# Kernel optimization log

Hardware: AMD Instinct MI355X
Metric: run time of the kernel (lower is better)

The kernel has to match this reference:

```python
import jax, jax.numpy as jnp
import numpy as np

EMB = 1024
HID = 1536
NE = 8


def setup_inputs() -> dict:
    key = jax.random.key(0)
    ks = jax.random.split(key, 8)
    B, N, E, H, ne = 4, 2048, EMB, HID, NE
    s = 1.0 / np.sqrt(E)
    sh = 1.0 / np.sqrt(H)
    return {
        "x": jax.random.normal(ks[0], (B, N, E), dtype=jnp.float32),
        "Wr": jax.random.uniform(ks[1], (E, ne), minval=-s, maxval=s, dtype=jnp.float32),
        "br": jax.random.uniform(ks[2], (ne,), minval=-s, maxval=s, dtype=jnp.float32),
        "W1": jax.random.uniform(ks[3], (ne, E, H), minval=-s, maxval=s, dtype=jnp.float32),
        "b1": jax.random.uniform(ks[4], (ne, H), minval=-s, maxval=s, dtype=jnp.float32),
        "W2": jax.random.uniform(ks[5], (ne, H, E), minval=-sh, maxval=sh, dtype=jnp.float32),
        "b2": jax.random.uniform(ks[6], (ne, E), minval=-sh, maxval=sh, dtype=jnp.float32),
        "k": 2,
    }


def reference(x, Wr, br, W1, b1, W2, b2, k):
    B, N, E = x.shape
    T = B * N
    ne = Wr.shape[1]
    flat = x.reshape(T, E)
    logits = flat @ Wr + br                      # [T, ne]
    _, topk_idx = jax.lax.top_k(logits, k)       # [T, k]
    # counts[t, e] = number of top-k slots of token t assigned to expert e
    counts = jax.nn.one_hot(topk_idx, ne, dtype=flat.dtype).sum(axis=1)  # [T, ne]
    out = jnp.zeros_like(flat)
    for e in range(ne):  # small fixed loop over experts (structurally distinct weights)
        h = jax.nn.gelu(flat @ W1[e] + b1[e], approximate=False)  # torch nn.GELU = exact erf
        y = h @ W2[e] + b2[e]
        out = out + counts[:, e:e + 1] * y
    out = out / k
    return out.reshape(B, N, E)
```

## Files before the change

kernel.cpp:

```cpp
#include <hip/hip_runtime.h>
#include <hip/hip_bf16.h>
#include <math.h>

#define T_TOK 8192
#define EMB   1024
#define HID   1536
#define NE    8
#define NBINB 64
#define BINTOK (T_TOK / NBINB)

typedef float  floatx4 __attribute__((ext_vector_type(4)));
typedef __bf16 bf16x8  __attribute__((ext_vector_type(8)));

#define WS_COUNTS   0
#define WS_OFFSETS  1024
#define WS_FLAGS    2048
#define WS_BHIST    4096
#define WS_TOKMAP   8192
#define WS_TOKLIST  270336
#define WS_YBUF     532480
#define WS_W1T      34086912
#define WS_W2T      59252736
#define WS_H        84418560
#define WS_NEEDED   135143424

__device__ __forceinline__ float eload(const void* p, size_t idx, bool f32) {
  return f32 ? ((const float*)p)[idx] : (float)(((const __bf16*)p)[idx]);
}

__device__ __forceinline__ void glds16(const void* g, void* l) {
  __builtin_amdgcn_global_load_lds(
      (const __attribute__((address_space(1))) unsigned int*)g,
      (__attribute__((address_space(3))) unsigned int*)l, 16, 0, 0);
}

__global__ __launch_bounds__(256)
void sniff_kernel(const void* p0, const void* p1, const void* p2, const void* p3,
                  const void* p4, const void* p5, const void* p6, int* flags) {
  const void* ps[7] = {p0, p1, p2, p3, p4, p5, p6};
  const int nelem[7] = {T_TOK * EMB, EMB * NE, NE, NE * EMB * HID, NE * HID, NE * HID * EMB, NE * EMB};
  int t = blockIdx.x;
  const unsigned* w = (const unsigned*)ps[t];
  int nw = nelem[t] / 2;
  if (nw > 2048) nw = 2048;
  __shared__ int s_pl, s_nz;
  if (threadIdx.x == 0) { s_pl = 0; s_nz = 0; }
  __syncthreads();
  int pl = 0, nz = 0;
  for (int i = threadIdx.x; i < nw; i += 256) {
    unsigned v = w[i];
    if (v == 0) continue;
    nz++;
    unsigned e = (v >> 23) & 0xFF;
    if (e >= 100 && e <= 150) pl++;
  }
  atomicAdd(&s_pl, pl);
  atomicAdd(&s_nz, nz);
  __syncthreads();
  if (threadIdx.x == 0) flags[t] = (2 * s_pl > s_nz) ? 1 : 0;
}

__global__ __launch_bounds__(256)
void logits_kernel(const void* __restrict__ x, const void* __restrict__ Wr,
                   const void* __restrict__ br, const int* __restrict__ kptr,
                   const int* __restrict__ flags, int* __restrict__ topk,
                   __bf16* __restrict__ xbf) {
  const bool xf32  = flags[0] != 0;
  const bool wrf32 = flags[1] != 0;
  const bool brf32 = flags[2] != 0;
  const int wave = threadIdx.x >> 6;
  const int lane = threadIdx.x & 63;
  const int t = blockIdx.x * 4 + wave;

  float xv[16];
  {
    size_t base = (size_t)t * EMB + lane * 16;
    if (xf32) {
      const float* g = (const float*)x + base;
#pragma unroll
      for (int j = 0; j < 16; ++j) xv[j] = g[j];
    } else {
      bf16x8 u = *(const bf16x8*)((const __bf16*)x + base);
      bf16x8 v = *(const bf16x8*)((const __bf16*)x + base + 8);
#pragma unroll
      for (int j = 0; j < 8; ++j) { xv[j] = (float)u[j]; xv[8 + j] = (float)v[j]; }
    }
  }
  {
    bf16x8 o0, o1;
#pragma unroll
    for (int j = 0; j < 8; ++j) { o0[j] = (__bf16)xv[j]; o1[j] = (__bf16)xv[8 + j]; }
    __bf16* xo = xbf + (size_t)t * EMB + lane * 16;
    *(bf16x8*)xo = o0;
    *(bf16x8*)(xo + 8) = o1;
  }
  float acc[NE];
#pragma unroll
  for (int e = 0; e < NE; ++e) acc[e] = 0.f;
  if (wrf32) {
#pragma unroll
    for (int j = 0; j < 16; ++j) {
      const float* wr = (const float*)Wr + (size_t)(lane * 16 + j) * NE;
#pragma unroll
      for (int e = 0; e < NE; ++e) acc[e] += xv[j] * wr[e];
    }
  } else {
#pragma unroll
    for (int j = 0; j < 16; ++j) {
      bf16x8 wr = *(const bf16x8*)((const __bf16*)Wr + (size_t)(lane * 16 + j) * NE);
#pragma unroll
      for (int e = 0; e < NE; ++e) acc[e] += xv[j] * (float)wr[e];
    }
  }
#pragma unroll
  for (int e = 0; e < NE; ++e) {
#pragma unroll
    for (int off = 32; off > 0; off >>= 1)
      acc[e] += __shfl_xor(acc[e], off, 64);
  }
  if (lane == 0) {
    int k = kptr[0];
    if (k < 1) k = 1; if (k > NE) k = NE;
    float lg[NE];
#pragma unroll
    for (int e = 0; e < NE; ++e) lg[e] = acc[e] + eload(br, e, brf32);
    for (int s = 0; s < k; ++s) {
      int bi = 0; float bv = lg[0];
#pragma unroll
      for (int e = 1; e < NE; ++e) { if (lg[e] > bv) { bv = lg[e]; bi = e; } }
      lg[bi] = -3.0e38f;
      topk[t * 8 + s] = bi;
    }
  }
}

__global__ __launch_bounds__(128)
void bin1_kernel(const int* __restrict__ topk, const int* __restrict__ kptr,
                 int* __restrict__ bhist) {
  __shared__ int lhist[NE];
  if (threadIdx.x < NE) lhist[threadIdx.x] = 0;
  __syncthreads();
  int k = kptr[0];
  if (k < 1) k = 1; if (k > NE) k = NE;
  const int t = blockIdx.x * BINTOK + threadIdx.x;
  for (int s = 0; s < k; ++s) atomicAdd(&lhist[topk[t * 8 + s] & 7], 1);
  __syncthreads();
  if (threadIdx.x < NE) bhist[blockIdx.x * NE + threadIdx.x] = lhist[threadIdx.x];
}

__global__ __launch_bounds__(256)
void scan_kernel(int* __restrict__ bhist, int* __restrict__ counts, int* __restrict__ offsets) {
  __shared__ int sh[NBINB * NE];
  __shared__ int scnt[NE];
  __shared__ int soff[NE + 1];
  const int tid = threadIdx.x;
  for (int i = tid; i < NBINB * NE; i += 256) sh[i] = bhist[i];
  __syncthreads();
  if (tid < NE) {
    int s = 0;
    for (int b = 0; b < NBINB; ++b) s += sh[b * NE + tid];
    scnt[tid] = s;
  }
  __syncthreads();
  if (tid == 0) {
    int s = 0;
    for (int e = 0; e < NE; ++e) { soff[e] = s; s += scnt[e]; }
    soff[NE] = s;
  }
  __syncthreads();
  if (tid < NE) {
    int run = soff[tid];
    for (int b = 0; b < NBINB; ++b) {
      int v = sh[b * NE + tid];
      sh[b * NE + tid] = run;
      run += v;
    }
  }
  __syncthreads();
  for (int i = tid; i < NBINB * NE; i += 256) bhist[i] = sh[i];
  if (tid < NE) counts[tid] = scnt[tid];
  if (tid < NE + 1) offsets[tid] = soff[tid];
}

__global__ __launch_bounds__(128)
void bin2_kernel(const int* __restrict__ bhist, const int* __restrict__ offsets,
                 const int* __restrict__ kptr,
                 int* __restrict__ tok_list, int* __restrict__ tokmap) {
  __shared__ int lbase[NE];
  __shared__ int lcnt[NE];
  if (threadIdx.x < NE) {
    lbase[threadIdx.x] = bhist[blockIdx.x * NE + threadIdx.x];
    lcnt[threadIdx.x] = 0;
  }
  __syncthreads();
  int k = kptr[0];
  if (k < 1) k = 1; if (k > NE) k = NE;
  const int t = blockIdx.x * BINTOK + threadIdx.x;
  for (int s = 0; s < k; ++s) {
    int e = tokmap[t * 8 + s] & 7;
    int pos = atomicAdd(&lcnt[e], 1);
    int grow = lbase[e] + pos;
    tok_list[e * T_TOK + (grow - offsets[e])] = t;
    tokmap[t * 8 + s] = (e << 16) | grow;
  }
}

__global__ __launch_bounds__(256)
void transpose2_kernel(const void* __restrict__ W1, const void* __restrict__ W2,
                       __bf16* __restrict__ w1t, __bf16* __restrict__ w2t,
                       const int* __restrict__ flags) {
  const int z = blockIdx.z;
  const void* in; __bf16* out; int K, N; bool f32;
  if (z < 8) { in = W1; out = w1t; K = EMB; N = HID; f32 = flags[3] != 0; }
  else       { in = W2; out = w2t; K = HID; N = EMB; f32 = flags[5] != 0; }
  if ((int)blockIdx.x * 64 >= N || (int)blockIdx.y * 64 >= K) return;
  __shared__ __bf16 tile[64][66];
  size_t eoff = (size_t)(z & 7) * (size_t)K * (size_t)N;
  const int n0 = blockIdx.x * 64;
  const int k0 = blockIdx.y * 64;
  const int tid = threadIdx.x;

  if (f32) {
    const int nn = (tid & 15) * 4;
    const int kr = tid >> 4;
#pragma unroll
    for (int p = 0; p < 4; ++p) {
      const int k = kr + p * 16;
      float4 v = *(const float4*)((const float*)in + eoff + (size_t)(k0 + k) * N + n0 + nn);
      tile[k][nn + 0] = (__bf16)v.x; tile[k][nn + 1] = (__bf16)v.y;
      tile[k][nn + 2] = (__bf16)v.z; tile[k][nn + 3] = (__bf16)v.w;
    }
  } else {
    const int nn = (tid & 7) * 8;
    const int kr = tid >> 3;
#pragma unroll
    for (int p = 0; p < 2; ++p) {
      const int k = kr + p * 32;
      bf16x8 v = *(const bf16x8*)((const __bf16*)in + eoff + (size_t)(k0 + k) * N + n0 + nn);
#pragma unroll
      for (int j = 0; j < 8; ++j) tile[k][nn + j] = v[j];
    }
  }
  __syncthreads();
  const int kk = (tid & 7) * 8;
  const int nr = tid >> 3;
#pragma unroll
  for (int p = 0; p < 2; ++p) {
    const int n = nr + p * 32;
    bf16x8 o;
#pragma unroll
    for (int j = 0; j < 8; ++j) o[j] = tile[kk + j][n];
    *(bf16x8*)(out + eoff + (size_t)(n0 + n) * K + k0 + kk) = o;
  }
}


__global__ __launch_bounds__(256, 4)
void gemm1_kernel(const __bf16* __restrict__ xbf, const __bf16* __restrict__ w1t,
                  const void* __restrict__ b1, const int* __restrict__ counts,
                  const int* __restrict__ offsets, const int* __restrict__ tok_list,
                  const int* __restrict__ flags, __bf16* __restrict__ hbuf) {
  const int flat = blockIdx.x;
  const int e   = flat & 7;
  const int idx = flat >> 3;
  const int g   = idx / 12;
  const int nT  = idx % 12;
  const int cnt = counts[e];
  const bool b1f32 = flags[4] != 0;

  __shared__ __align__(16) __bf16 As[128 * 64];
  __shared__ __align__(16) __bf16 Bs[128 * 64];

  const int wave = threadIdx.x >> 6;
  const int lane = threadIdx.x & 63;
  const int lrow = lane >> 3;
  const int cgs  = (lane & 7) ^ lrow;

  int Rst[4];
#pragma unroll
  for (int q = 0; q < 4; ++q) Rst[q] = (q * 4 + wave) * 8 + lrow;

  const __bf16* pB[4];
#pragma unroll
  for (int q = 0; q < 4; ++q)
    pB[q] = w1t + ((size_t)e * HID + nT * 128 + Rst[q]) * EMB + cgs * 8;

  const int wm = (wave & 1) * 64;
  const int wn = (wave >> 1) * 64;
  const int fr = lane & 15;
  const int fc = lane >> 4;
  int aOff0[4], aOff1[4], bOff0[4], bOff1[4];
#pragma unroll
  for (int i = 0; i < 4; ++i) {
    int R = wm + i * 16 + fr;
    aOff0[i] = R * 128 + (((fc)     ^ (R & 7)) << 4);
    aOff1[i] = R * 128 + (((fc + 4) ^ (R & 7)) << 4);
  }
#pragma unroll
  for (int j = 0; j < 4; ++j) {
    int R = wn + j * 16 + fr;
    bOff0[j] = R * 128 + (((fc)     ^ (R & 7)) << 4);
    bOff1[j] = R * 128 + (((fc + 4) ^ (R & 7)) << 4);
  }

  const int colBase = nT * 128 + wn + fr;
  float bv[4];
#pragma unroll
  for (int j = 0; j < 4; ++j) bv[j] = eload(b1, (size_t)e * HID + colBase + j * 16, b1f32);

  for (int mT = g; mT * 128 < cnt; mT += 16) {
    const __bf16* pA[4];
#pragma unroll
    for (int q = 0; q < 4; ++q) {
      const int tok = tok_list[e * T_TOK + mT * 128 + Rst[q]];
      pA[q] = xbf + (size_t)tok * EMB + cgs * 8;
    }

    floatx4 acc[4][4];
#pragma unroll
    for (int i = 0; i < 4; ++i)
#pragma unroll
      for (int j = 0; j < 4; ++j) acc[i][j] = (floatx4){0.f, 0.f, 0.f, 0.f};

    for (int kb = 0; kb < EMB / 64; ++kb) {
      __syncthreads();
#pragma unroll
      for (int q = 0; q < 4; ++q) glds16(pA[q] + (size_t)kb * 64, As + (q * 4 + wave) * 512);
#pragma unroll
      for (int q = 0; q < 4; ++q) glds16(pB[q] + (size_t)kb * 64, Bs + (q * 4 + wave) * 512);
      __syncthreads();
      bf16x8 af[4], bfr[4];
#pragma unroll
      for (int i = 0; i < 4; ++i) af[i]  = *(const bf16x8*)((const char*)As + aOff0[i]);
#pragma unroll
      for (int j = 0; j < 4; ++j) bfr[j] = *(const bf16x8*)((const char*)Bs + bOff0[j]);
#pragma unroll
      for (int i = 0; i < 4; ++i)
#pragma unroll
        for (int j = 0; j < 4; ++j)
          acc[i][j] = __builtin_amdgcn_mfma_f32_16x16x32_bf16(af[i], bfr[j], acc[i][j], 0, 0, 0);
#pragma unroll
      for (int i = 0; i < 4; ++i) af[i]  = *(const bf16x8*)((const char*)As + aOff1[i]);
#pragma unroll
      for (int j = 0; j < 4; ++j) bfr[j] = *(const bf16x8*)((const char*)Bs + bOff1[j]);
#pragma unroll
      for (int i = 0; i < 4; ++i)
#pragma unroll
        for (int j = 0; j < 4; ++j)
          acc[i][j] = __builtin_amdgcn_mfma_f32_16x16x32_bf16(af[i], bfr[j], acc[i][j], 0, 0, 0);
    }

    const int hBase = offsets[e] + mT * 128;
#pragma unroll
    for (int i = 0; i < 4; ++i) {
      const int rowLoc = wm + i * 16 + fc * 4;
#pragma unroll
      for (int r = 0; r < 4; ++r) {
        const int row = rowLoc + r;
        if (mT * 128 + row < cnt) {
          __bf16* hp = hbuf + (size_t)(hBase + row) * HID + colBase;
#pragma unroll
          for (int j = 0; j < 4; ++j) {
            float v = acc[i][j][r] + bv[j];
            float gl = 0.5f * v * (1.0f + erff(v * 0.70710678118654752f));
            hp[j * 16] = (__bf16)gl;
          }
        }
      }
    }
  }
}

__global__ __launch_bounds__(256, 4)
void gemm2_kernel(const __bf16* __restrict__ hbuf, const __bf16* __restrict__ w2t,
                  const void* __restrict__ b2, const int* __restrict__ counts,
                  const int* __restrict__ offsets, const int* __restrict__ flags,
                  __bf16* __restrict__ ybuf) {
  const int flat = blockIdx.x;
  const int e   = flat & 7;
  const int idx = flat >> 3;
  const int g   = idx >> 3;
  const int nT  = idx & 7;
  const int cnt = counts[e];
  const bool b2f32 = flags[6] != 0;

  __shared__ __align__(16) __bf16 As[128 * 64];
  __shared__ __align__(16) __bf16 Bs[128 * 64];

  const int wave = threadIdx.x >> 6;
  const int lane = threadIdx.x & 63;
  const int lrow = lane >> 3;
  const int cgs  = (lane & 7) ^ lrow;

  int Rst[4];
#pragma unroll
  for (int q = 0; q < 4; ++q) Rst[q] = (q * 4 + wave) * 8 + lrow;

  const __bf16* pB[4];
#pragma unroll
  for (int q = 0; q < 4; ++q)
    pB[q] = w2t + ((size_t)e * EMB + nT * 128 + Rst[q]) * HID + cgs * 8;

  const int wm = (wave & 1) * 64;
  const int wn = (wave >> 1) * 64;
  const int fr = lane & 15;
  const int fc = lane >> 4;
  int aOff0[4], aOff1[4], bOff0[4], bOff1[4];
#pragma unroll
  for (int i = 0; i < 4; ++i) {
    int R = wm + i * 16 + fr;
    aOff0[i] = R * 128 + (((fc)     ^ (R & 7)) << 4);
    aOff1[i] = R * 128 + (((fc + 4) ^ (R & 7)) << 4);
  }
#pragma unroll
  for (int j = 0; j < 4; ++j) {
    int R = wn + j * 16 + fr;
    bOff0[j] = R * 128 + (((fc)     ^ (R & 7)) << 4);
    bOff1[j] = R * 128 + (((fc + 4) ^ (R & 7)) << 4);
  }

  const int colBase = nT * 128 + wn + fr;
  float bv[4];
#pragma unroll
  for (int j = 0; j < 4; ++j) bv[j] = eload(b2, (size_t)e * EMB + colBase + j * 16, b2f32);

  for (int mT = g; mT * 128 < cnt; mT += 16) {
    const int rowBase = offsets[e] + mT * 128;
    const __bf16* pA[4];
#pragma unroll
    for (int q = 0; q < 4; ++q)
      pA[q] = hbuf + (size_t)(rowBase + Rst[q]) * HID + cgs * 8;

    floatx4 acc[4][4];
#pragma unroll
    for (int i = 0; i < 4; ++i)
#pragma unroll
      for (int j = 0; j < 4; ++j) acc[i][j] = (floatx4){0.f, 0.f, 0.f, 0.f};

    for (int kb = 0; kb < HID / 64; ++kb) {
      __syncthreads();
#pragma unroll
      for (int q = 0; q < 4; ++q) glds16(pA[q] + (size_t)kb * 64, As + (q * 4 + wave) * 512);
#pragma unroll
      for (int q = 0; q < 4; ++q) glds16(pB[q] + (size_t)kb * 64, Bs + (q * 4 + wave) * 512);
      __syncthreads();
      bf16x8 af[4], bfr[4];
#pragma unroll
      for (int i = 0; i < 4; ++i) af[i]  = *(const bf16x8*)((const char*)As + aOff0[i]);
#pragma unroll
      for (int j = 0; j < 4; ++j) bfr[j] = *(const bf16x8*)((const char*)Bs + bOff0[j]);
#pragma unroll
      for (int i = 0; i < 4; ++i)
#pragma unroll
        for (int j = 0; j < 4; ++j)
          acc[i][j] = __builtin_amdgcn_mfma_f32_16x16x32_bf16(af[i], bfr[j], acc[i][j], 0, 0, 0);
#pragma unroll
      for (int i = 0; i < 4; ++i) af[i]  = *(const bf16x8*)((const char*)As + aOff1[i]);
#pragma unroll
      for (int j = 0; j < 4; ++j) bfr[j] = *(const bf16x8*)((const char*)Bs + bOff1[j]);
#pragma unroll
      for (int i = 0; i < 4; ++i)
#pragma unroll
        for (int j = 0; j < 4; ++j)
          acc[i][j] = __builtin_amdgcn_mfma_f32_16x16x32_bf16(af[i], bfr[j], acc[i][j], 0, 0, 0);
    }

#pragma unroll
    for (int i = 0; i < 4; ++i) {
      const int rowLoc = wm + i * 16 + fc * 4;
#pragma unroll
      for (int r = 0; r < 4; ++r) {
        const int row = rowLoc + r;
        if (mT * 128 + row < cnt) {
          __bf16* yp = ybuf + (size_t)(rowBase + row) * EMB + colBase;
#pragma unroll
          for (int j = 0; j < 4; ++j)
            yp[j * 16] = (__bf16)(acc[i][j][r] + bv[j]);
        }
      }
    }
  }
}

__global__ __launch_bounds__(256)
void combine_kernel(const __bf16* __restrict__ ybuf, const int* __restrict__ tokmap,
                    const int* __restrict__ kptr, const int* __restrict__ flags,
                    void* __restrict__ out) {
  const bool f32 = flags[0] != 0;
  const int wave = threadIdx.x >> 6;
  const int lane = threadIdx.x & 63;
  const int t = blockIdx.x * 4 + wave;
  int k = kptr[0];
  if (k < 1) k = 1; if (k > NE) k = NE;
  const float invk = 1.0f / (float)k;
  int rows[NE];
  for (int s = 0; s < k; ++s) rows[s] = tokmap[t * 8 + s] & 0xFFFF;
#pragma unroll
  for (int c = 0; c < 2; ++c) {
    const int i = c * 512 + lane * 8;
    float a[8];
#pragma unroll
    for (int j = 0; j < 8; ++j) a[j] = 0.f;
    for (int s = 0; s < k; ++s) {
      bf16x8 y = *(const bf16x8*)(ybuf + (size_t)rows[s] * EMB + i);
#pragma unroll
      for (int j = 0; j < 8; ++j) a[j] += (float)y[j];
    }
    if (f32) {
      float* op = (float*)out + (size_t)t * EMB + i;
      float4 u = {a[0] * invk, a[1] * invk, a[2] * invk, a[3] * invk};
      float4 v = {a[4] * invk, a[5] * invk, a[6] * invk, a[7] * invk};
      *(float4*)op = u;
      *(float4*)(op + 4) = v;
    } else {
      bf16x8 o;
#pragma unroll
      for (int j = 0; j < 8; ++j) o[j] = (__bf16)(a[j] * invk);
      *(bf16x8*)((__bf16*)out + (size_t)t * EMB + i) = o;
    }
  }
}

extern "C" void kernel_launch(void* const* d_in, const int* in_sizes, int n_in,
                              void* d_out, int out_size, void* d_ws, size_t ws_size,
                              hipStream_t stream) {
  (void)in_sizes; (void)n_in; (void)out_size;
  if (ws_size < (size_t)WS_NEEDED) return;

  const void* x  = d_in[0];
  const void* Wr = d_in[1];
  const void* br = d_in[2];
  const void* W1 = d_in[3];
  const void* b1 = d_in[4];
  const void* W2 = d_in[5];
  const void* b2 = d_in[6];
  const int* kptr = (const int*)d_in[7];

  char* ws = (char*)d_ws;
  int*    counts   = (int*)(ws + WS_COUNTS);
  int*    offsets  = (int*)(ws + WS_OFFSETS);
  int*    flags    = (int*)(ws + WS_FLAGS);
  int*    bhist    = (int*)(ws + WS_BHIST);
  int*    tokmap   = (int*)(ws + WS_TOKMAP);
  int*    tok_list = (int*)(ws + WS_TOKLIST);
  __bf16* ybuf     = (__bf16*)(ws + WS_YBUF);
  __bf16* xbf      = (__bf16*)(ws + WS_YBUF);
  __bf16* w1t      = (__bf16*)(ws + WS_W1T);
  __bf16* w2t      = (__bf16*)(ws + WS_W2T);
  __bf16* hbuf     = (__bf16*)(ws + WS_H);

  hipMemsetAsync(ws + WS_TOKLIST, 0, NE * T_TOK * 4, stream);

  sniff_kernel<<<dim3(7), 256, 0, stream>>>(x, Wr, br, W1, b1, W2, b2, flags);

  transpose2_kernel<<<dim3(HID / 64, HID / 64, 16), 256, 0, stream>>>(W1, W2, w1t, w2t, flags);

  logits_kernel<<<dim3(T_TOK / 4), 256, 0, stream>>>(x, Wr, br, kptr, flags, tokmap, xbf);
  bin1_kernel<<<dim3(NBINB), 128, 0, stream>>>(tokmap, kptr, bhist);
  scan_kernel<<<dim3(1), 256, 0, stream>>>(bhist, counts, offsets);
  bin2_kernel<<<dim3(NBINB), 128, 0, stream>>>(bhist, offsets, kptr, tok_list, tokmap);

  gemm1_kernel<<<dim3(8 * 16 * 12), 256, 0, stream>>>(
      xbf, w1t, b1, counts, offsets, tok_list, flags, hbuf);
  gemm2_kernel<<<dim3(8 * 16 * 8), 256, 0, stream>>>(
      hbuf, w2t, b2, counts, offsets, flags, ybuf);

  combine_kernel<<<dim3(T_TOK / 4), 256, 0, stream>>>(ybuf, tokmap, kptr, flags, d_out);
}
```

Before: 368.5 us.

## Fuse weight transpose with logits, collapse binning into one single-block kernel

Merges the weight transpose/convert kernel and the router logits kernel into one launch partitioned by block index. The three binning kernels (histogram, scan, scatter) and the memset become a single 1024-thread block that assigns per-expert positions directly and zero-pads only the tail of each expert list. Combine now adds the expert offset to recover global rows. It also vectorizes the fp32 x load. This cuts launch count and removes the transpose-to-logits serialization, but binning on one block is serial over 8192 tokens and the atomic order makes slot assignment nondeterministic.

```diff
diff --git a/kernel.cpp b/kernel.cpp
--- a/kernel.cpp
+++ b/kernel.cpp
@@ -6,8 +6,6 @@
 #define EMB   1024
 #define HID   1536
 #define NE    8
-#define NBINB 64
-#define BINTOK (T_TOK / NBINB)
 
 typedef float  floatx4 __attribute__((ext_vector_type(4)));
 typedef __bf16 bf16x8  __attribute__((ext_vector_type(8)));
@@ -15,7 +13,6 @@
 #define WS_COUNTS   0
 #define WS_OFFSETS  1024
 #define WS_FLAGS    2048
-#define WS_BHIST    4096
 #define WS_TOKMAP   8192
 #define WS_TOKLIST  270336
 #define WS_YBUF     532480
@@ -61,16 +58,70 @@
 }
 
 __global__ __launch_bounds__(256)
-void logits_kernel(const void* __restrict__ x, const void* __restrict__ Wr,
-                   const void* __restrict__ br, const int* __restrict__ kptr,
-                   const int* __restrict__ flags, int* __restrict__ topk,
-                   __bf16* __restrict__ xbf) {
+void prep_kernel(const void* __restrict__ W1, const void* __restrict__ W2,
+                 __bf16* __restrict__ w1t, __bf16* __restrict__ w2t,
+                 const void* __restrict__ x, const void* __restrict__ Wr,
+                 const void* __restrict__ br, const int* __restrict__ kptr,
+                 const int* __restrict__ flags, int* __restrict__ topk,
+                 __bf16* __restrict__ xbf) {
+  __shared__ __bf16 tile[64][66];
+  const int bid = blockIdx.x;
+  const int tid = threadIdx.x;
+
+  if (bid < 6144) {
+    const void* in; __bf16* out; int K, N; bool f32; int e, nb, kb;
+    if (bid < 3072) {
+      in = W1; out = w1t; K = EMB; N = HID; f32 = flags[3] != 0;
+      e = bid / 384; int rem = bid % 384; nb = rem % 24; kb = rem / 24;
+    } else {
+      in = W2; out = w2t; K = HID; N = EMB; f32 = flags[5] != 0;
+      int w = bid - 3072; e = w / 384; int rem = w % 384; nb = rem % 16; kb = rem / 16;
+    }
+    size_t eoff = (size_t)e * (size_t)K * (size_t)N;
+    const int n0 = nb * 64;
+    const int k0 = kb * 64;
+
+    if (f32) {
+      const int nn = (tid & 15) * 4;
+      const int kr = tid >> 4;
+#pragma unroll
+      for (int p = 0; p < 4; ++p) {
+        const int k = kr + p * 16;
+        float4 v = *(const float4*)((const float*)in + eoff + (size_t)(k0 + k) * N + n0 + nn);
+        tile[k][nn + 0] = (__bf16)v.x; tile[k][nn + 1] = (__bf16)v.y;
+        tile[k][nn + 2] = (__bf16)v.z; tile[k][nn + 3] = (__bf16)v.w;
+      }
+    } else {
+      const int nn = (tid & 7) * 8;
+      const int kr = tid >> 3;
+#pragma unroll
+      for (int p = 0; p < 2; ++p) {
+        const int k = kr + p * 32;
+        bf16x8 v = *(const bf16x8*)((const __bf16*)in + eoff + (size_t)(k0 + k) * N + n0 + nn);
+#pragma unroll
+        for (int j = 0; j < 8; ++j) tile[k][nn + j] = v[j];
+      }
+    }
+    __syncthreads();
+    const int kk = (tid & 7) * 8;
+    const int nr = tid >> 3;
+#pragma unroll
+    for (int p = 0; p < 2; ++p) {
+      const int n = nr + p * 32;
+      bf16x8 o;
+#pragma unroll
+      for (int j = 0; j < 8; ++j) o[j] = tile[kk + j][n];
+      *(bf16x8*)(out + eoff + (size_t)(n0 + n) * K + k0 + kk) = o;
+    }
+    return;
+  }
+
   const bool xf32  = flags[0] != 0;
   const bool wrf32 = flags[1] != 0;
   const bool brf32 = flags[2] != 0;
-  const int wave = threadIdx.x >> 6;
-  const int lane = threadIdx.x & 63;
-  const int t = blockIdx.x * 4 + wave;
+  const int wave = tid >> 6;
+  const int lane = tid & 63;
+  const int t = (bid - 6144) * 4 + wave;
 
   float xv[16];
   {
@@ -78,7 +129,10 @@
     if (xf32) {
       const float* g = (const float*)x + base;
 #pragma unroll
-      for (int j = 0; j < 16; ++j) xv[j] = g[j];
+      for (int c = 0; c < 4; ++c) {
+        float4 v = *(const float4*)(g + c * 4);
+        xv[c * 4 + 0] = v.x; xv[c * 4 + 1] = v.y; xv[c * 4 + 2] = v.z; xv[c * 4 + 3] = v.w;
+      }
     } else {
       bf16x8 u = *(const bf16x8*)((const __bf16*)x + base);
       bf16x8 v = *(const bf16x8*)((const __bf16*)x + base + 8);
@@ -134,123 +188,38 @@
   }
 }
 
-__global__ __launch_bounds__(128)
-void bin1_kernel(const int* __restrict__ topk, const int* __restrict__ kptr,
-                 int* __restrict__ bhist) {
-  __shared__ int lhist[NE];
-  if (threadIdx.x < NE) lhist[threadIdx.x] = 0;
+__global__ __launch_bounds__(1024)
+void bin_kernel(const int* __restrict__ kptr, int* __restrict__ tokmap,
+                int* __restrict__ tok_list, int* __restrict__ counts,
+                int* __restrict__ offsets) {
+  __shared__ int lcnt[NE];
+  __shared__ int soff[NE + 1];
+  const int tid = threadIdx.x;
+  if (tid < NE) lcnt[tid] = 0;
   __syncthreads();
   int k = kptr[0];
   if (k < 1) k = 1; if (k > NE) k = NE;
-  const int t = blockIdx.x * BINTOK + threadIdx.x;
-  for (int s = 0; s < k; ++s) atomicAdd(&lhist[topk[t * 8 + s] & 7], 1);
-  __syncthreads();
-  if (threadIdx.x < NE) bhist[blockIdx.x * NE + threadIdx.x] = lhist[threadIdx.x];
-}
-
-__global__ __launch_bounds__(256)
-void scan_kernel(int* __restrict__ bhist, int* __restrict__ counts, int* __restrict__ offsets) {
-  __shared__ int sh[NBINB * NE];
-  __shared__ int scnt[NE];
-  __shared__ int soff[NE + 1];
-  const int tid = threadIdx.x;
-  for (int i = tid; i < NBINB * NE; i += 256) sh[i] = bhist[i];
-  __syncthreads();
-  if (tid < NE) {
-    int s = 0;
-    for (int b = 0; b < NBINB; ++b) s += sh[b * NE + tid];
-    scnt[tid] = s;
+  for (int t = tid; t < T_TOK; t += 1024) {
+    for (int s = 0; s < k; ++s) {
+      int e = tokmap[t * 8 + s] & 7;
+      int pos = atomicAdd(&lcnt[e], 1);
+      tok_list[e * T_TOK + pos] = t;
+      tokmap[t * 8 + s] = (e << 16) | pos;
+    }
   }
   __syncthreads();
   if (tid == 0) {
     int s = 0;
-    for (int e = 0; e < NE; ++e) { soff[e] = s; s += scnt[e]; }
+    for (int e = 0; e < NE; ++e) { soff[e] = s; s += lcnt[e]; }
     soff[NE] = s;
   }
   __syncthreads();
-  if (tid < NE) {
-    int run = soff[tid];
-    for (int b = 0; b < NBINB; ++b) {
-      int v = sh[b * NE + tid];
-      sh[b * NE + tid] = run;
-      run += v;
-    }
-  }
-  __syncthreads();
-  for (int i = tid; i < NBINB * NE; i += 256) bhist[i] = sh[i];
-  if (tid < NE) counts[tid] = scnt[tid];
-  if (tid < NE + 1) offsets[tid] = soff[tid];
-}
-
-__global__ __launch_bounds__(128)
-void bin2_kernel(const int* __restrict__ bhist, const int* __restrict__ offsets,
-                 const int* __restrict__ kptr,
-                 int* __restrict__ tok_list, int* __restrict__ tokmap) {
-  __shared__ int lbase[NE];
-  __shared__ int lcnt[NE];
-  if (threadIdx.x < NE) {
-    lbase[threadIdx.x] = bhist[blockIdx.x * NE + threadIdx.x];
-    lcnt[threadIdx.x] = 0;
-  }
-  __syncthreads();
-  int k = kptr[0];
-  if (k < 1) k = 1; if (k > NE) k = NE;
-  const int t = blockIdx.x * BINTOK + threadIdx.x;
-  for (int s = 0; s < k; ++s) {
-    int e = tokmap[t * 8 + s] & 7;
-    int pos = atomicAdd(&lcnt[e], 1);
-    int grow = lbase[e] + pos;
-    tok_list[e * T_TOK + (grow - offsets[e])] = t;
-    tokmap[t * 8 + s] = (e << 16) | grow;
-  }
-}
-
-__global__ __launch_bounds__(256)
-void transpose2_kernel(const void* __restrict__ W1, const void* __restrict__ W2,
-                       __bf16* __restrict__ w1t, __bf16* __restrict__ w2t,
-                       const int* __restrict__ flags) {
-  const int z = blockIdx.z;
-  const void* in; __bf16* out; int K, N; bool f32;
-  if (z < 8) { in = W1; out = w1t; K = EMB; N = HID; f32 = flags[3] != 0; }
-  else       { in = W2; out = w2t; K = HID; N = EMB; f32 = flags[5] != 0; }
-  if ((int)blockIdx.x * 64 >= N || (int)blockIdx.y * 64 >= K) return;
-  __shared__ __bf16 tile[64][66];
-  size_t eoff = (size_t)(z & 7) * (size_t)K * (size_t)N;
-  const int n0 = blockIdx.x * 64;
-  const int k0 = blockIdx.y * 64;
-  const int tid = threadIdx.x;
-
-  if (f32) {
-    const int nn = (tid & 15) * 4;
-    const int kr = tid >> 4;
-#pragma unroll
-    for (int p = 0; p < 4; ++p) {
-      const int k = kr + p * 16;
-      float4 v = *(const float4*)((const float*)in + eoff + (size_t)(k0 + k) * N + n0 + nn);
-      tile[k][nn + 0] = (__bf16)v.x; tile[k][nn + 1] = (__bf16)v.y;
-      tile[k][nn + 2] = (__bf16)v.z; tile[k][nn + 3] = (__bf16)v.w;
-    }
-  } else {
-    const int nn = (tid & 7) * 8;
-    const int kr = tid >> 3;
-#pragma unroll
-    for (int p = 0; p < 2; ++p) {
-      const int k = kr + p * 32;
-      bf16x8 v = *(const bf16x8*)((const __bf16*)in + eoff + (size_t)(k0 + k) * N + n0 + nn);
-#pragma unroll
-      for (int j = 0; j < 8; ++j) tile[k][nn + j] = v[j];
-    }
-  }
-  __syncthreads();
-  const int kk = (tid & 7) * 8;
-  const int nr = tid >> 3;
-#pragma unroll
-  for (int p = 0; p < 2; ++p) {
-    const int n = nr + p * 32;
-    bf16x8 o;
-#pragma unroll
-    for (int j = 0; j < 8; ++j) o[j] = tile[kk + j][n];
-    *(bf16x8*)(out + eoff + (size_t)(n0 + n) * K + k0 + kk) = o;
+  if (tid < NE) counts[tid] = lcnt[tid];
+  if (tid <= NE) offsets[tid] = soff[tid];
+  for (int e = 0; e < NE; ++e) {
+    const int c = lcnt[e];
+    const int end = (c + 127) & ~127;
+    for (int i = c + tid; i < end; i += 1024) tok_list[e * T_TOK + i] = 0;
   }
 }
 
@@ -484,8 +453,8 @@
 
 __global__ __launch_bounds__(256)
 void combine_kernel(const __bf16* __restrict__ ybuf, const int* __restrict__ tokmap,
-                    const int* __restrict__ kptr, const int* __restrict__ flags,
-                    void* __restrict__ out) {
+                    const int* __restrict__ offsets, const int* __restrict__ kptr,
+                    const int* __restrict__ flags, void* __restrict__ out) {
   const bool f32 = flags[0] != 0;
   const int wave = threadIdx.x >> 6;
   const int lane = threadIdx.x & 63;
@@ -494,7 +463,10 @@
   if (k < 1) k = 1; if (k > NE) k = NE;
   const float invk = 1.0f / (float)k;
   int rows[NE];
-  for (int s = 0; s < k; ++s) rows[s] = tokmap[t * 8 + s] & 0xFFFF;
+  for (int s = 0; s < k; ++s) {
+    int m = tokmap[t * 8 + s];
+    rows[s] = offsets[(m >> 16) & 7] + (m & 0xFFFF);
+  }
 #pragma unroll
   for (int c = 0; c < 2; ++c) {
     const int i = c * 512 + lane * 8;
@@ -540,7 +512,6 @@
   int*    counts   = (int*)(ws + WS_COUNTS);
   int*    offsets  = (int*)(ws + WS_OFFSETS);
   int*    flags    = (int*)(ws + WS_FLAGS);
-  int*    bhist    = (int*)(ws + WS_BHIST);
   int*    tokmap   = (int*)(ws + WS_TOKMAP);
   int*    tok_list = (int*)(ws + WS_TOKLIST);
   __bf16* ybuf     = (__bf16*)(ws + WS_YBUF);
@@ -549,21 +520,17 @@
   __bf16* w2t      = (__bf16*)(ws + WS_W2T);
   __bf16* hbuf     = (__bf16*)(ws + WS_H);
 
-  hipMemsetAsync(ws + WS_TOKLIST, 0, NE * T_TOK * 4, stream);
-
   sniff_kernel<<<dim3(7), 256, 0, stream>>>(x, Wr, br, W1, b1, W2, b2, flags);
 
-  transpose2_kernel<<<dim3(HID / 64, HID / 64, 16), 256, 0, stream>>>(W1, W2, w1t, w2t, flags);
-
-  logits_kernel<<<dim3(T_TOK / 4), 256, 0, stream>>>(x, Wr, br, kptr, flags, tokmap, xbf);
-  bin1_kernel<<<dim3(NBINB), 128, 0, stream>>>(tokmap, kptr, bhist);
-  scan_kernel<<<dim3(1), 256, 0, stream>>>(bhist, counts, offsets);
-  bin2_kernel<<<dim3(NBINB), 128, 0, stream>>>(bhist, offsets, kptr, tok_list, tokmap);
+  prep_kernel<<<dim3(6144 + T_TOK / 4), 256, 0, stream>>>(
+      W1, W2, w1t, w2t, x, Wr, br, kptr, flags, tokmap, xbf);
+
+  bin_kernel<<<dim3(1), 1024, 0, stream>>>(kptr, tokmap, tok_list, counts, offsets);
 
   gemm1_kernel<<<dim3(8 * 16 * 12), 256, 0, stream>>>(
       xbf, w1t, b1, counts, offsets, tok_list, flags, hbuf);
   gemm2_kernel<<<dim3(8 * 16 * 8), 256, 0, stream>>>(
       hbuf, w2t, b2, counts, offsets, flags, ybuf);
 
-  combine_kernel<<<dim3(T_TOK / 4), 256, 0, stream>>>(ybuf, tokmap, kptr, flags, d_out);
-}
+  combine_kernel<<<dim3(T_TOK / 4), 256, 0, stream>>>(ybuf, tokmap, offsets, kptr, flags, d_out);
+}
```

After: 370.9 us. Within noise of the previous version (+0.6%).
